# Kernel tuning notes

Measured on AMD Instinct MI355X. Metric: run time of the kernel, lower is better.

The kernel has to match this reference:

```python
import jax, jax.numpy as jnp
import numpy as np

B, IN, OUT = 2048, 512, 512

def setup_inputs() -> dict:
    key = jax.random.key(0)
    k1, k2, k3 = jax.random.split(key, 3)
    x = jax.random.normal(k1, (B, IN), dtype=jnp.float32)
    dilation_weight = jax.random.normal(k2, (OUT, IN), dtype=jnp.float32)
    erosion_weight = jax.random.normal(k3, (OUT, IN), dtype=jnp.float32)
    return {"x": x, "dilation_weight": dilation_weight, "erosion_weight": erosion_weight}

def reference(x, dilation_weight, erosion_weight):
    # tropical (max-plus) matmul: [B,1,IN] + [OUT,IN] -> max over IN -> [B,OUT]
    dilation = jnp.max(x[:, None, :] + dilation_weight, axis=2)
    # (min-minus): [B,1,IN] - [OUT,IN] -> min over IN -> [B,OUT]
    erosion = jnp.min(x[:, None, :] - erosion_weight, axis=2)
    return dilation + erosion
```

## Files before the change

### kernel.cpp

```cpp
#include <hip/hip_runtime.h>
#include <math.h>

#define BM 64
#define BN 64
#define BK 32
#define B_TOT 2048
#define IN_TOT 512
#define OUT_TOT 512
#define LSTR 36
#define NTILES (IN_TOT / BK)

__global__ __launch_bounds__(256) void morph_kernel(
    const float* __restrict__ x,
    const float* __restrict__ wdil,
    const float* __restrict__ wero,
    float* __restrict__ out)
{
    __shared__ float sx[2][BM * LSTR];
    __shared__ float sd[2][BN * LSTR];
    __shared__ float se[2][BN * LSTR];

    const int tid = (int)threadIdx.x;
    const int tx = tid & 15;
    const int ty = tid >> 4;

    const int brow0 = (int)blockIdx.y * BM;
    const int bcol0 = (int)blockIdx.x * BN;

    const int srow = tid >> 3;
    const int sj   = tid & 7;

    const size_t xoff0 = (size_t)(brow0 + srow) * IN_TOT + sj * 4;
    const size_t xoff1 = xoff0 + (size_t)32 * IN_TOT;
    const size_t woff0 = (size_t)(bcol0 + srow) * IN_TOT + sj * 4;
    const size_t woff1 = woff0 + (size_t)32 * IN_TOT;

    const int l0 = srow * LSTR + sj * 4;
    const int l1 = (srow + 32) * LSTR + sj * 4;

    float4 rx0, rx1, rd0, rd1, re0, re1;

    rx0 = *(const float4*)(x    + xoff0);
    rx1 = *(const float4*)(x    + xoff1);
    rd0 = *(const float4*)(wdil + woff0);
    rd1 = *(const float4*)(wdil + woff1);
    re0 = *(const float4*)(wero + woff0);
    re1 = *(const float4*)(wero + woff1);

    *(float4*)&sx[0][l0] = rx0;
    *(float4*)&sx[0][l1] = rx1;
    *(float4*)&sd[0][l0] = rd0;
    *(float4*)&sd[0][l1] = rd1;
    *(float4*)&se[0][l0] = re0;
    *(float4*)&se[0][l1] = re1;

    __syncthreads();

    float dil[4][4], ero[4][4];
#pragma unroll
    for (int m = 0; m < 4; ++m)
#pragma unroll
        for (int n = 0; n < 4; ++n) {
            dil[m][n] = -INFINITY;
            ero[m][n] =  INFINITY;
        }

#pragma unroll 1
    for (int t = 0; t < NTILES; ++t) {
        const int cur = t & 1;

        if (t + 1 < NTILES) {
            const int k0 = (t + 1) * BK;
            rx0 = *(const float4*)(x    + xoff0 + k0);
            rx1 = *(const float4*)(x    + xoff1 + k0);
            rd0 = *(const float4*)(wdil + woff0 + k0);
            rd1 = *(const float4*)(wdil + woff1 + k0);
            re0 = *(const float4*)(wero + woff0 + k0);
            re1 = *(const float4*)(wero + woff1 + k0);
        }

        const float* __restrict__ xb = sx[cur];
        const float* __restrict__ db = sd[cur];
        const float* __restrict__ eb = se[cur];

#pragma unroll
        for (int kk = 0; kk < BK; kk += 4) {
            float4 xv[4], dv[4], ev[4];
#pragma unroll
            for (int m = 0; m < 4; ++m)
                xv[m] = *(const float4*)&xb[(ty + 16 * m) * LSTR + kk];
#pragma unroll
            for (int n = 0; n < 4; ++n) {
                dv[n] = *(const float4*)&db[(tx + 16 * n) * LSTR + kk];
                ev[n] = *(const float4*)&eb[(tx + 16 * n) * LSTR + kk];
            }
#pragma unroll
            for (int m = 0; m < 4; ++m)
#pragma unroll
                for (int n = 0; n < 4; ++n) {
                    float a0 = xv[m].x + dv[n].x;
                    float a1 = xv[m].y + dv[n].y;
                    float a2 = xv[m].z + dv[n].z;
                    float a3 = xv[m].w + dv[n].w;
                    dil[m][n] = fmaxf(fmaxf(a0, a1), dil[m][n]);
                    dil[m][n] = fmaxf(fmaxf(a2, a3), dil[m][n]);
                    float s0 = xv[m].x - ev[n].x;
                    float s1 = xv[m].y - ev[n].y;
                    float s2 = xv[m].z - ev[n].z;
                    float s3 = xv[m].w - ev[n].w;
                    ero[m][n] = fminf(fminf(s0, s1), ero[m][n]);
                    ero[m][n] = fminf(fminf(s2, s3), ero[m][n]);
                }
        }

        if (t + 1 < NTILES) {
            const int nxt = cur ^ 1;
            *(float4*)&sx[nxt][l0] = rx0;
            *(float4*)&sx[nxt][l1] = rx1;
            *(float4*)&sd[nxt][l0] = rd0;
            *(float4*)&sd[nxt][l1] = rd1;
            *(float4*)&se[nxt][l0] = re0;
            *(float4*)&se[nxt][l1] = re1;
        }
        __syncthreads();
    }

#pragma unroll
    for (int m = 0; m < 4; ++m) {
        const int r = brow0 + ty + 16 * m;
#pragma unroll
        for (int n = 0; n < 4; ++n) {
            const int c = bcol0 + tx + 16 * n;
            out[(size_t)r * OUT_TOT + c] = dil[m][n] + ero[m][n];
        }
    }
}

extern "C" void kernel_launch(void* const* d_in, const int* in_sizes, int n_in,
                              void* d_out, int out_size, void* d_ws, size_t ws_size,
                              hipStream_t stream)
{
    const float* x  = (const float*)d_in[0];
    const float* wd = (const float*)d_in[1];
    const float* we = (const float*)d_in[2];
    float* out = (float*)d_out;

    dim3 grid(OUT_TOT / BN, B_TOT / BM);
    dim3 block(256);
    hipLaunchKernelGGL(morph_kernel, grid, block, 0, stream, x, wd, we, out);
}
```

Baseline: 69.99 us.

## Use wave-uniform scalar x loads with swizzled LDS weight tiles

```diff
diff --git a/kernel.cpp b/kernel.cpp
--- a/kernel.cpp
+++ b/kernel.cpp
@@ -1,139 +1,111 @@
 #include <hip/hip_runtime.h>
 #include <math.h>
 
-#define BM 64
-#define BN 64
-#define BK 32
 #define B_TOT 2048
 #define IN_TOT 512
 #define OUT_TOT 512
-#define LSTR 36
-#define NTILES (IN_TOT / BK)
+#define BK 32
+#define NT (IN_TOT / BK)
+#define RPW 8
+#define WAVES 4
+#define RPB (RPW * WAVES)
+#define COLS 64
 
-__global__ __launch_bounds__(256) void morph_kernel(
+__global__ __launch_bounds__(256, 2) void morph_kernel(
     const float* __restrict__ x,
     const float* __restrict__ wdil,
     const float* __restrict__ wero,
     float* __restrict__ out)
 {
-    __shared__ float sx[2][BM * LSTR];
-    __shared__ float sd[2][BN * LSTR];
-    __shared__ float se[2][BN * LSTR];
+    __shared__ float wd_s[2][COLS * BK];
+    __shared__ float we_s[2][COLS * BK];
 
-    const int tid = (int)threadIdx.x;
-    const int tx = tid & 15;
-    const int ty = tid >> 4;
+    const int tid  = (int)threadIdx.x;
+    const int lane = tid & 63;
+    const int wav  = tid >> 6;
 
-    const int brow0 = (int)blockIdx.y * BM;
-    const int bcol0 = (int)blockIdx.x * BN;
+    const int col0 = (int)blockIdx.x * COLS;
+    const int row0 = (int)blockIdx.y * RPB;
+    const int wrow = __builtin_amdgcn_readfirstlane(row0 + wav * RPW);
 
-    const int srow = tid >> 3;
-    const int sj   = tid & 7;
+    const float* xp = x + (size_t)wrow * IN_TOT;
 
-    const size_t xoff0 = (size_t)(brow0 + srow) * IN_TOT + sj * 4;
-    const size_t xoff1 = xoff0 + (size_t)32 * IN_TOT;
-    const size_t woff0 = (size_t)(bcol0 + srow) * IN_TOT + sj * 4;
-    const size_t woff1 = woff0 + (size_t)32 * IN_TOT;
+    int soff[2];
+#pragma unroll
+    for (int i = 0; i < 2; ++i) {
+        int s = i * 256 + tid;
+        int c = s >> 3;
+        int cs = (s & 7) ^ (c & 7);
+        soff[i] = (col0 + c) * IN_TOT + cs * 4;
+    }
+    const int lw0 = tid * 4;
+    const int lw1 = 1024 + tid * 4;
 
-    const int l0 = srow * LSTR + sj * 4;
-    const int l1 = (srow + 32) * LSTR + sj * 4;
+    float dil[RPW], ero[RPW];
+#pragma unroll
+    for (int r = 0; r < RPW; ++r) { dil[r] = -INFINITY; ero[r] = INFINITY; }
 
-    float4 rx0, rx1, rd0, rd1, re0, re1;
-
-    rx0 = *(const float4*)(x    + xoff0);
-    rx1 = *(const float4*)(x    + xoff1);
-    rd0 = *(const float4*)(wdil + woff0);
-    rd1 = *(const float4*)(wdil + woff1);
-    re0 = *(const float4*)(wero + woff0);
-    re1 = *(const float4*)(wero + woff1);
-
-    *(float4*)&sx[0][l0] = rx0;
-    *(float4*)&sx[0][l1] = rx1;
-    *(float4*)&sd[0][l0] = rd0;
-    *(float4*)&sd[0][l1] = rd1;
-    *(float4*)&se[0][l0] = re0;
-    *(float4*)&se[0][l1] = re1;
-
+    {
+        float4 a0 = *(const float4*)(wdil + soff[0]);
+        float4 a1 = *(const float4*)(wdil + soff[1]);
+        float4 b0 = *(const float4*)(wero + soff[0]);
+        float4 b1 = *(const float4*)(wero + soff[1]);
+        *(float4*)&wd_s[0][lw0] = a0;
+        *(float4*)&wd_s[0][lw1] = a1;
+        *(float4*)&we_s[0][lw0] = b0;
+        *(float4*)&we_s[0][lw1] = b1;
+    }
     __syncthreads();
 
-    float dil[4][4], ero[4][4];
-#pragma unroll
-    for (int m = 0; m < 4; ++m)
-#pragma unroll
-        for (int n = 0; n < 4; ++n) {
-            dil[m][n] = -INFINITY;
-            ero[m][n] =  INFINITY;
+    const int lbase = lane << 5;
+    const int lxor  = (lane & 7) << 2;
+
+#pragma unroll 1
+    for (int t = 0; t < NT; ++t) {
+        const int buf = t & 1;
+        const bool pf = (t + 1 < NT);
+        float4 a0, a1, b0, b1;
+        if (pf) {
+            const int kb = (t + 1) * BK;
+            a0 = *(const float4*)(wdil + soff[0] + kb);
+            a1 = *(const float4*)(wdil + soff[1] + kb);
+            b0 = *(const float4*)(wero + soff[0] + kb);
+            b1 = *(const float4*)(wero + soff[1] + kb);
         }
 
-#pragma unroll 1
-    for (int t = 0; t < NTILES; ++t) {
-        const int cur = t & 1;
+        const float* wdp = &wd_s[buf][0];
+        const float* wep = &we_s[buf][0];
+        const float* xt  = xp + t * BK;
 
-        if (t + 1 < NTILES) {
-            const int k0 = (t + 1) * BK;
-            rx0 = *(const float4*)(x    + xoff0 + k0);
-            rx1 = *(const float4*)(x    + xoff1 + k0);
-            rd0 = *(const float4*)(wdil + woff0 + k0);
-            rd1 = *(const float4*)(wdil + woff1 + k0);
-            re0 = *(const float4*)(wero + woff0 + k0);
-            re1 = *(const float4*)(wero + woff1 + k0);
+#pragma unroll
+        for (int c = 0; c < 8; ++c) {
+            const int wo = lbase + ((c << 2) ^ lxor);
+            float4 wd4 = *(const float4*)(wdp + wo);
+            float4 we4 = *(const float4*)(wep + wo);
+#pragma unroll
+            for (int r = 0; r < RPW; ++r) {
+                float4 xv = *(const float4*)(xt + r * IN_TOT + (c << 2));
+                dil[r] = fmaxf(fmaxf(xv.x + wd4.x, xv.y + wd4.y),
+                          fmaxf(fmaxf(xv.z + wd4.z, xv.w + wd4.w), dil[r]));
+                ero[r] = fminf(fminf(xv.x - we4.x, xv.y - we4.y),
+                          fminf(fminf(xv.z - we4.z, xv.w - we4.w), ero[r]));
+            }
         }
 
-        const float* __restrict__ xb = sx[cur];
-        const float* __restrict__ db = sd[cur];
-        const float* __restrict__ eb = se[cur];
-
-#pragma unroll
-        for (int kk = 0; kk < BK; kk += 4) {
-            float4 xv[4], dv[4], ev[4];
-#pragma unroll
-            for (int m = 0; m < 4; ++m)
-                xv[m] = *(const float4*)&xb[(ty + 16 * m) * LSTR + kk];
-#pragma unroll
-            for (int n = 0; n < 4; ++n) {
-                dv[n] = *(const float4*)&db[(tx + 16 * n) * LSTR + kk];
-                ev[n] = *(const float4*)&eb[(tx + 16 * n) * LSTR + kk];
-            }
-#pragma unroll
-            for (int m = 0; m < 4; ++m)
-#pragma unroll
-                for (int n = 0; n < 4; ++n) {
-                    float a0 = xv[m].x + dv[n].x;
-                    float a1 = xv[m].y + dv[n].y;
-                    float a2 = xv[m].z + dv[n].z;
-                    float a3 = xv[m].w + dv[n].w;
-                    dil[m][n] = fmaxf(fmaxf(a0, a1), dil[m][n]);
-                    dil[m][n] = fmaxf(fmaxf(a2, a3), dil[m][n]);
-                    float s0 = xv[m].x - ev[n].x;
-                    float s1 = xv[m].y - ev[n].y;
-                    float s2 = xv[m].z - ev[n].z;
-                    float s3 = xv[m].w - ev[n].w;
-                    ero[m][n] = fminf(fminf(s0, s1), ero[m][n]);
-                    ero[m][n] = fminf(fminf(s2, s3), ero[m][n]);
-                }
-        }
-
-        if (t + 1 < NTILES) {
-            const int nxt = cur ^ 1;
-            *(float4*)&sx[nxt][l0] = rx0;
-            *(float4*)&sx[nxt][l1] = rx1;
-            *(float4*)&sd[nxt][l0] = rd0;
-            *(float4*)&sd[nxt][l1] = rd1;
-            *(float4*)&se[nxt][l0] = re0;
-            *(float4*)&se[nxt][l1] = re1;
+        if (pf) {
+            const int nb = buf ^ 1;
+            *(float4*)&wd_s[nb][lw0] = a0;
+            *(float4*)&wd_s[nb][lw1] = a1;
+            *(float4*)&we_s[nb][lw0] = b0;
+            *(float4*)&we_s[nb][lw1] = b1;
         }
         __syncthreads();
     }
 
+    float* op = out + (size_t)wrow * OUT_TOT + col0 + lane;
 #pragma unroll
-    for (int m = 0; m < 4; ++m) {
-        const int r = brow0 + ty + 16 * m;
-#pragma unroll
-        for (int n = 0; n < 4; ++n) {
-            const int c = bcol0 + tx + 16 * n;
-            out[(size_t)r * OUT_TOT + c] = dil[m][n] + ero[m][n];
-        }
-    }
+    for (int r = 0; r < RPW; ++r)
+        op[r * OUT_TOT] = dil[r] + ero[r];
 }
 
 extern "C" void kernel_launch(void* const* d_in, const int* in_sizes, int n_in,
@@ -145,7 +117,7 @@
     const float* we = (const float*)d_in[2];
     float* out = (float*)d_out;
 
-    dim3 grid(OUT_TOT / BN, B_TOT / BM);
+    dim3 grid(OUT_TOT / COLS, B_TOT / RPB);
     dim3 block(256);
     hipLaunchKernelGGL(morph_kernel, grid, block, 0, stream, x, wd, we, out);
 }
```

Result: slower. 87.09 us (+24.4%).
